# Kernel tuning notes

Measured on AMD Instinct MI355X. Metric: run time of the kernel, lower is better.

The kernel has to match this reference:

```python
import jax, jax.numpy as jnp
import numpy as np

N = 100000   # nodes
E = 1600000  # edges (avg degree 16)
F = 128      # num_features
H = 128      # hidden_channels
L = 3        # mp_layers
C = 40       # num_classes
EPS = 1e-5   # BatchNorm eps


def setup_inputs() -> dict:
    key = jax.random.key(0)
    ks = jax.random.split(key, 6)
    x = jax.random.normal(ks[0], (N, F), dtype=jnp.float32)
    edge_index = jax.random.randint(ks[1], (2, E), 0, N, dtype=jnp.int64)
    # GCNConv weights (F==H so all layers share shape), PyG-style lin + bias
    Ws = jax.random.normal(ks[2], (L, H, H), dtype=jnp.float32) * 0.05
    bs = jnp.zeros((L, H), dtype=jnp.float32)
    # BatchNorm affine params
    gammas = jnp.ones((L, H), dtype=jnp.float32)
    betas = jnp.zeros((L, H), dtype=jnp.float32)
    # output head: skip-concat dim = F + L*H
    W_out = jax.random.normal(ks[3], (F + L * H, C), dtype=jnp.float32) * 0.05
    b_out = jnp.zeros((C,), dtype=jnp.float32)
    return {"x": x, "Ws": Ws, "bs": bs, "gammas": gammas, "betas": betas,
            "W_out": W_out, "b_out": b_out, "edge_index": edge_index}


def reference(x, Ws, bs, gammas, betas, W_out, b_out, edge_index):
    src, dst = edge_index[0], edge_index[1]
    n = x.shape[0]
    # GCN symmetric normalization with self-loops (PyG gcn_norm, add_self_loops=True)
    deg = jax.ops.segment_sum(jnp.ones(src.shape[0], x.dtype), dst, num_segments=n) + 1.0
    dinv = jax.lax.rsqrt(deg)
    edge_norm = (dinv[src] * dinv[dst])[:, None]   # [E,1]
    self_norm = (dinv * dinv)[:, None]             # [N,1] self-loop contribution

    outs = [x]
    h = x
    for i in range(L):
        hw = h @ Ws[i]                                                   # [N,H]
        msg = hw[src] * edge_norm                                        # gather [E,H]
        agg = jax.ops.segment_sum(msg, dst, num_segments=n)              # scatter-add
        agg = agg + hw * self_norm + bs[i]
        # BatchNorm1d in training mode (batch stats, biased variance)
        mu = agg.mean(axis=0)
        var = agg.var(axis=0)
        h = gammas[i] * (agg - mu) * jax.lax.rsqrt(var + EPS) + betas[i]
        outs.append(h)  # dropout p=0.0 -> identity; skip=True collects each layer

    xcat = jnp.concatenate(outs, axis=1)  # [N, F + L*H]
    return xcat @ W_out + b_out
```

## Files before the change

### kernel.cpp

```cpp
#include <hip/hip_runtime.h>

#define NN 100000
#define NE 1600000
#define HD 128
#define NL 3
#define NC 40
#define NCP 48

#define NBK 196
#define NPB 512
#define BSH 9
#define CAP 9216
#define PCAP 13312
#define EPB 6400
#define NBINBLK 250

typedef unsigned int u32;
typedef unsigned short u16;
typedef __attribute__((ext_vector_type(8))) short short8;
typedef __attribute__((ext_vector_type(4))) float f32x4;

__device__ __forceinline__ float b2f(u16 h){
    union{u32 u; float f;} v; v.u = ((u32)h) << 16; return v.f;
}
__device__ __forceinline__ u16 f2b(float f){
    union{float f; u32 u;} v; v.f = f;
    u32 u = v.u;
    u32 r = (u + 0x7FFFu + ((u >> 16) & 1u)) >> 16;
    return (u16)r;
}

__global__ void k_conv_w(const float* __restrict__ Ws, u16* __restrict__ wt,
                         int* __restrict__ gcur, float* __restrict__ stats,
                         u16* __restrict__ hwzero, const float* __restrict__ Wout,
                         u16* __restrict__ woutt){
    int i = blockIdx.x * blockDim.x + threadIdx.x;
    if (i < NBK) gcur[i] = 0;
    if (i < NL * 2 * HD) stats[i] = 0.f;
    if (i < HD) hwzero[i] = 0;
    if (i < (NL + 1) * NCP * HD){
        int li = i / (NCP * HD);
        int r = i % (NCP * HD);
        int n = r / HD;
        int k = r % HD;
        woutt[i] = (n < NC) ? f2b(Wout[(size_t)(li * HD + k) * NC + n]) : (u16)0;
    }
    if (i >= NL * HD * HD) return;
    int l = i / (HD * HD);
    int r = i % (HD * HD);
    int n = r / HD;
    int k = r % HD;
    wt[i] = f2b(Ws[l * HD * HD + k * HD + n]);
}

__launch_bounds__(256)
__global__ void k_bin(const int* __restrict__ src, const int* __restrict__ dst,
                      int* __restrict__ gcur, u32* __restrict__ bb){
    __shared__ int hist[NBK];
    __shared__ int lbase[NBK];
    __shared__ int gbase[NBK];
    __shared__ int cur[NBK];
    __shared__ int wsum[4];
    __shared__ uint2 stage[EPB];
    int tid = threadIdx.x;
    int e0 = blockIdx.x * EPB;
    for (int i = tid; i < NBK; i += 256) hist[i] = 0;
    __syncthreads();
    for (int k = tid; k < EPB; k += 256){
        int d = dst[e0 + k];
        atomicAdd(&hist[d >> BSH], 1);
    }
    __syncthreads();
    {
        int v = (tid < NBK) ? hist[tid] : 0;
        int lane = tid & 63, w = tid >> 6;
        int incl = v;
        #pragma unroll
        for (int dlt = 1; dlt < 64; dlt <<= 1){
            int t = __shfl_up(incl, dlt);
            if (lane >= dlt) incl += t;
        }
        if (lane == 63) wsum[w] = incl;
        __syncthreads();
        if (tid == 0){
            int run = 0;
            #pragma unroll
            for (int j = 0; j < 4; j++){ int t = wsum[j]; wsum[j] = run; run += t; }
        }
        __syncthreads();
        int excl = wsum[w] + incl - v;
        if (tid < NBK){ lbase[tid] = excl; cur[tid] = excl; }
    }
    __syncthreads();
    if (tid < NBK) gbase[tid] = atomicAdd(&gcur[tid], hist[tid]);
    __syncthreads();
    for (int k = tid; k < EPB; k += 256){
        int s = src[e0 + k], d = dst[e0 + k];
        int pos = atomicAdd(&cur[d >> BSH], 1);
        stage[pos] = make_uint2((u32)s, (u32)d);
    }
    __syncthreads();
    for (int k = tid; k < EPB; k += 256){
        uint2 sd = stage[k];
        int b = (int)(sd.y >> BSH);
        int g = gbase[b] + (k - lbase[b]);
        if (g < CAP) bb[(size_t)b * CAP + g] = sd.x | ((sd.y & (NPB - 1)) << 17);
    }
}

__launch_bounds__(512)
__global__ void k_csr(const int* __restrict__ gcur, const u32* __restrict__ bb,
                      int* __restrict__ csr_src, int* __restrict__ offs,
                      int* __restrict__ oend, float* __restrict__ dinv){
    __shared__ int hist[NPB];
    __shared__ int cur[NPB];
    __shared__ int wsum[8];
    __shared__ int totp_s;
    __shared__ int lcsr[PCAP];
    int tid = threadIdx.x;
    int b = blockIdx.x;
    int cnt_b = gcur[b]; if (cnt_b > CAP) cnt_b = CAP;
    const u32* eb = bb + (size_t)b * CAP;
    hist[tid] = 0;
    __syncthreads();
    for (int k = tid; k < cnt_b; k += 512)
        atomicAdd(&hist[eb[k] >> 17], 1);
    __syncthreads();
    int cnt = hist[tid];
    int ps = (1 + cnt + 7) & ~7;
    int lane = tid & 63, w = tid >> 6;
    int incl = ps;
    #pragma unroll
    for (int dlt = 1; dlt < 64; dlt <<= 1){
        int t = __shfl_up(incl, dlt);
        if (lane >= dlt) incl += t;
    }
    if (lane == 63) wsum[w] = incl;
    __syncthreads();
    if (tid == 0){
        int run = 0;
        #pragma unroll
        for (int j = 0; j < 8; j++){ int t = wsum[j]; wsum[j] = run; run += t; }
        totp_s = run;
    }
    __syncthreads();
    int excl = wsum[w] + incl - ps;
    int n = b * NPB + tid;
    offs[n] = b * PCAP + excl;
    oend[n] = b * PCAP + excl + ps;
    if (n < NN) dinv[n] = rsqrtf((float)(cnt + 1));
    cur[tid] = excl + 1;
    int totp = totp_s;
    __syncthreads();
    for (int k = tid; k < totp; k += 512) lcsr[k] = NN;
    __syncthreads();
    lcsr[excl] = (n < NN) ? n : NN;
    __syncthreads();
    for (int k = tid; k < cnt_b; k += 512){
        u32 sd = eb[k];
        int pos = atomicAdd(&cur[sd >> 17], 1);
        lcsr[pos] = (int)(sd & 0x1FFFFu);
    }
    __syncthreads();
    for (int k = tid; k < totp; k += 512)
        csr_src[b * PCAP + k] = lcsr[k];
}

__launch_bounds__(256)
__global__ void k_convgemm(const float* __restrict__ x, const u16* __restrict__ wt,
                           const u16* __restrict__ woutt, const float* __restrict__ bout,
                           const float* __restrict__ dinv, u16* __restrict__ hw,
                           float* __restrict__ out){
    __shared__ u16 wlds[HD * HD];
    __shared__ u16 wolds[NCP * HD];
    __shared__ float bl[NC];
    int tid = threadIdx.x;
    {
        const uint4* g = reinterpret_cast<const uint4*>(wt);
        #pragma unroll
        for (int i = 0; i < 8; i++){
            int lin16 = tid + 256 * i;
            uint4 v = g[lin16];
            int c = lin16 >> 4;
            int addr16 = lin16 ^ (c & 7);
            reinterpret_cast<uint4*>(wlds)[addr16] = v;
        }
    }
    {
        const uint4* g = reinterpret_cast<const uint4*>(woutt);
        #pragma unroll
        for (int i = 0; i < 3; i++){
            int lin16 = tid + 256 * i;
            uint4 v = g[lin16];
            int c = lin16 >> 4;
            int addr16 = lin16 ^ (c & 7);
            reinterpret_cast<uint4*>(wolds)[addr16] = v;
        }
    }
    if (tid < NC) bl[tid] = bout[tid];
    __syncthreads();

    int wv = tid >> 6, lane = tid & 63;
    int row_base = blockIdx.x * 64 + wv * 16;
    int arow = row_base + (lane & 15);
    if (arow >= NN) arow = NN - 1;
    int koff = (lane >> 4) * 8;

    f32x4 accW[8];
    f32x4 accH[3];
    #pragma unroll
    for (int t = 0; t < 8; t++) accW[t] = (f32x4){0.f, 0.f, 0.f, 0.f};
    #pragma unroll
    for (int t = 0; t < 3; t++) accH[t] = (f32x4){0.f, 0.f, 0.f, 0.f};

    #pragma unroll
    for (int kk = 0; kk < 4; kk++){
        int fb = kk * 32 + koff;
        const float4* xr = reinterpret_cast<const float4*>(x + (size_t)arow * HD + fb);
        float4 v0 = xr[0];
        float4 v1 = xr[1];
        short8 a;
        a[0] = (short)f2b(v0.x); a[1] = (short)f2b(v0.y);
        a[2] = (short)f2b(v0.z); a[3] = (short)f2b(v0.w);
        a[4] = (short)f2b(v1.x); a[5] = (short)f2b(v1.y);
        a[6] = (short)f2b(v1.z); a[7] = (short)f2b(v1.w);
        #pragma unroll
        for (int ct = 0; ct < 8; ct++){
            int c = ct * 16 + (lane & 15);
            int addr16 = (c * 16 + kk * 4 + (koff >> 3)) ^ (c & 7);
            short8 b = *reinterpret_cast<const short8*>(wlds + addr16 * 8);
            accW[ct] = __builtin_amdgcn_mfma_f32_16x16x32_bf16(a, b, accW[ct], 0, 0, 0);
        }
        #pragma unroll
        for (int ht = 0; ht < 3; ht++){
            int c = ht * 16 + (lane & 15);
            int addr16 = (c * 16 + kk * 4 + (koff >> 3)) ^ (c & 7);
            short8 b = *reinterpret_cast<const short8*>(wolds + addr16 * 8);
            accH[ht] = __builtin_amdgcn_mfma_f32_16x16x32_bf16(a, b, accH[ht], 0, 0, 0);
        }
    }

    int drow = row_base + (lane >> 4) * 4;
    int dcol = lane & 15;
    float dv[4];
    #pragma unroll
    for (int r = 0; r < 4; r++){
        int rr = drow + r;
        dv[r] = dinv[rr < NN ? rr : NN - 1];
    }
    #pragma unroll
    for (int ct = 0; ct < 8; ct++){
        #pragma unroll
        for (int r = 0; r < 4; r++){
            int rr = drow + r;
            if (rr < NN) hw[rr * HD + ct * 16 + dcol] = f2b(accW[ct][r] * dv[r]);
        }
    }
    #pragma unroll
    for (int ht = 0; ht < 3; ht++){
        int col = ht * 16 + dcol;
        if (col < NC){
            float bv = bl[col];
            #pragma unroll
            for (int r = 0; r < 4; r++){
                int rr = drow + r;
                if (rr < NN) out[(size_t)rr * NC + col] = bv + accH[ht][r];
            }
        }
    }
}

template<bool DO_HW>
__launch_bounds__(256)
__global__ void k_gemmbn(const u16* __restrict__ agg, const float* __restrict__ sums,
                         const float* __restrict__ gamma, const float* __restrict__ beta,
                         const u16* __restrict__ wt, const u16* __restrict__ woutt,
                         const float* __restrict__ dinv, u16* __restrict__ hw,
                         float* __restrict__ out){
    __shared__ u16 wlds[HD * HD];
    __shared__ u16 wolds[NCP * HD];
    __shared__ float Al[HD];
    __shared__ float Cl[HD];
    int tid = threadIdx.x;
    if (DO_HW){
        const uint4* g = reinterpret_cast<const uint4*>(wt);
        #pragma unroll
        for (int i = 0; i < 8; i++){
            int lin16 = tid + 256 * i;
            uint4 v = g[lin16];
            int c = lin16 >> 4;
            int addr16 = lin16 ^ (c & 7);
            reinterpret_cast<uint4*>(wlds)[addr16] = v;
        }
    }
    {
        const uint4* g = reinterpret_cast<const uint4*>(woutt);
        #pragma unroll
        for (int i = 0; i < 3; i++){
            int lin16 = tid + 256 * i;
            uint4 v = g[lin16];
            int c = lin16 >> 4;
            int addr16 = lin16 ^ (c & 7);
            reinterpret_cast<uint4*>(wolds)[addr16] = v;
        }
    }
    if (tid < HD){
        float mu = sums[tid] / (float)NN;
        float var = sums[HD + tid] / (float)NN - mu * mu;
        float inv = rsqrtf(var + 1e-5f);
        float a = gamma[tid] * inv;
        Al[tid] = a;
        Cl[tid] = beta[tid] - mu * a;
    }
    __syncthreads();

    int wv = tid >> 6, lane = tid & 63;
    int row_base = blockIdx.x * 64 + wv * 16;
    int arow = row_base + (lane & 15);
    if (arow >= NN) arow = NN - 1;
    int koff = (lane >> 4) * 8;

    f32x4 accW[8];
    f32x4 accH[3];
    #pragma unroll
    for (int t = 0; t < 8; t++) accW[t] = (f32x4){0.f, 0.f, 0.f, 0.f};
    #pragma unroll
    for (int t = 0; t < 3; t++) accH[t] = (f32x4){0.f, 0.f, 0.f, 0.f};

    #pragma unroll
    for (int kk = 0; kk < 4; kk++){
        int fb = kk * 32 + koff;
        short8 raw = *reinterpret_cast<const short8*>(agg + (size_t)arow * HD + fb);
        f32x4 A0 = *reinterpret_cast<const f32x4*>(&Al[fb]);
        f32x4 A1 = *reinterpret_cast<const f32x4*>(&Al[fb + 4]);
        f32x4 C0 = *reinterpret_cast<const f32x4*>(&Cl[fb]);
        f32x4 C1 = *reinterpret_cast<const f32x4*>(&Cl[fb + 4]);
        short8 a;
        #pragma unroll
        for (int j = 0; j < 4; j++){
            a[j]     = (short)f2b(b2f((u16)raw[j])     * A0[j] + C0[j]);
            a[j + 4] = (short)f2b(b2f((u16)raw[j + 4]) * A1[j] + C1[j]);
        }
        if (DO_HW){
            #pragma unroll
            for (int ct = 0; ct < 8; ct++){
                int c = ct * 16 + (lane & 15);
                int addr16 = (c * 16 + kk * 4 + (koff >> 3)) ^ (c & 7);
                short8 b = *reinterpret_cast<const short8*>(wlds + addr16 * 8);
                accW[ct] = __builtin_amdgcn_mfma_f32_16x16x32_bf16(a, b, accW[ct], 0, 0, 0);
            }
        }
        #pragma unroll
        for (int ht = 0; ht < 3; ht++){
            int c = ht * 16 + (lane & 15);
            int addr16 = (c * 16 + kk * 4 + (koff >> 3)) ^ (c & 7);
            short8 b = *reinterpret_cast<const short8*>(wolds + addr16 * 8);
            accH[ht] = __builtin_amdgcn_mfma_f32_16x16x32_bf16(a, b, accH[ht], 0, 0, 0);
        }
    }

    int drow = row_base + (lane >> 4) * 4;
    int dcol = lane & 15;
    if (DO_HW){
        float dv[4];
        #pragma unroll
        for (int r = 0; r < 4; r++){
            int rr = drow + r;
            dv[r] = dinv[rr < NN ? rr : NN - 1];
        }
        #pragma unroll
        for (int ct = 0; ct < 8; ct++){
            #pragma unroll
            for (int r = 0; r < 4; r++){
                int rr = drow + r;
                if (rr < NN) hw[rr * HD + ct * 16 + dcol] = f2b(accW[ct][r] * dv[r]);
            }
        }
    }
    #pragma unroll
    for (int ht = 0; ht < 3; ht++){
        int col = ht * 16 + dcol;
        if (col < NC){
            #pragma unroll
            for (int r = 0; r < 4; r++){
                int rr = drow + r;
                if (rr < NN) out[(size_t)rr * NC + col] += accH[ht][r];
            }
        }
    }
}

__launch_bounds__(256)
__global__ void k_agg(const u16* __restrict__ hw, const int* __restrict__ offs,
                      const int* __restrict__ oend, const int* __restrict__ csr_src,
                      const float* __restrict__ dinv, const float* __restrict__ bias,
                      u16* __restrict__ agg, float* __restrict__ sums){
    __shared__ float redS[4][HD];
    __shared__ float redQ[4][HD];
    int tid = threadIdx.x;
    int lane = tid & 63;
    int wv = tid >> 6;
    int f0 = lane * 2;
    float b0 = bias[f0], b1 = bias[f0 + 1];
    float s0 = 0.f, s1 = 0.f, q0 = 0.f, q1 = 0.f;
    int n0 = (blockIdx.x * 4 + wv) * 16;
    const u32* hw32 = reinterpret_cast<const u32*>(hw);

    for (int k = 0; k < 16; k++){
        int n = n0 + k;
        if (n >= NN) break;
        float a0 = 0.f, a1 = 0.f, c0 = 0.f, c1 = 0.f;
        int e = offs[n], e1 = oend[n];
        int rem = e1 - e;
        while (rem > 0){
            int win = rem < 64 ? rem : 64;
            int idxv = csr_src[e + lane];
            int nch = win >> 3;
            u32 va[8], vb[8];

            #pragma unroll
            for (int j = 0; j < 8; j++){
                u32 uid = (u32)__builtin_amdgcn_readlane(idxv, j);
                va[j] = hw32[(size_t)(uid << 6) + (u32)lane];
            }
            for (int c = 1; c < nch; c++){
                if (c & 1){
                    #pragma unroll
                    for (int j = 0; j < 8; j++){
                        u32 uid = (u32)__builtin_amdgcn_readlane(idxv, c * 8 + j);
                        vb[j] = hw32[(size_t)(uid << 6) + (u32)lane];
                    }
                    #pragma unroll
                    for (int j = 0; j < 8; j++){
                        union{u32 u; float f;} L, H;
                        L.u = va[j] << 16; H.u = va[j] & 0xFFFF0000u;
                        a0 += L.f; a1 += H.f;
                    }
                } else {
                    #pragma unroll
                    for (int j = 0; j < 8; j++){
                        u32 uid = (u32)__builtin_amdgcn_readlane(idxv, c * 8 + j);
                        va[j] = hw32[(size_t)(uid << 6) + (u32)lane];
                    }
                    #pragma unroll
                    for (int j = 0; j < 8; j++){
                        union{u32 u; float f;} L, H;
                        L.u = vb[j] << 16; H.u = vb[j] & 0xFFFF0000u;
                        c0 += L.f; c1 += H.f;
                    }
                }
            }
            if (nch & 1){
                #pragma unroll
                for (int j = 0; j < 8; j++){
                    union{u32 u; float f;} L, H;
                    L.u = va[j] << 16; H.u = va[j] & 0xFFFF0000u;
                    a0 += L.f; a1 += H.f;
                }
            } else {
                #pragma unroll
                for (int j = 0; j < 8; j++){
                    union{u32 u; float f;} L, H;
                    L.u = vb[j] << 16; H.u = vb[j] & 0xFFFF0000u;
                    c0 += L.f; c1 += H.f;
                }
            }
            e += win; rem -= win;
        }
        float di = dinv[n];
        a0 = (a0 + c0) * di + b0;
        a1 = (a1 + c1) * di + b1;
        u32 o = ((u32)f2b(a1) << 16) | (u32)f2b(a0);
        *reinterpret_cast<u32*>(agg + (size_t)n * HD + f0) = o;
        s0 += a0; s1 += a1; q0 += a0 * a0; q1 += a1 * a1;
    }

    redS[wv][f0] = s0; redS[wv][f0 + 1] = s1;
    redQ[wv][f0] = q0; redQ[wv][f0 + 1] = q1;
    __syncthreads();
    if (tid < HD){
        float ts = redS[0][tid] + redS[1][tid] + redS[2][tid] + redS[3][tid];
        float tq = redQ[0][tid] + redQ[1][tid] + redQ[2][tid] + redQ[3][tid];
        atomicAdd(&sums[tid], ts);
        atomicAdd(&sums[HD + tid], tq);
    }
}

extern "C" void kernel_launch(void* const* d_in, const int* in_sizes, int n_in,
                              void* d_out, int out_size, void* d_ws, size_t ws_size,
                              hipStream_t stream){
    const float* x      = (const float*)d_in[0];
    const float* Ws     = (const float*)d_in[1];
    const float* bs     = (const float*)d_in[2];
    const float* gammas = (const float*)d_in[3];
    const float* betas  = (const float*)d_in[4];
    const float* W_out  = (const float*)d_in[5];
    const float* b_out  = (const float*)d_in[6];
    const int*   ei     = (const int*)d_in[7];
    const int* src = ei;
    const int* dst = ei + NE;
    float* out = (float*)d_out;

    char* ws = (char*)d_ws;
    size_t off = 0;
    auto alloc = [&](size_t bytes) -> char* {
        char* p = ws + off;
        off += (bytes + 255) & ~(size_t)255;
        return p;
    };
    u16*   hw       = (u16*)alloc((size_t)(NN + 1) * HD * 2);
    u16*   aggb     = (u16*)alloc((size_t)NN * HD * 2);
    u16*   wt       = (u16*)alloc((size_t)NL * HD * HD * 2);
    u16*   woutt    = (u16*)alloc((size_t)(NL + 1) * NCP * HD * 2);
    float* dinv     = (float*)alloc((size_t)NN * 4);
    int*   offs     = (int*)alloc((size_t)(NBK * NPB) * 4);
    int*   oend     = (int*)alloc((size_t)(NBK * NPB) * 4);
    int*   gcur     = (int*)alloc((size_t)NBK * 4);
    int*   csr_src  = (int*)alloc(((size_t)NBK * PCAP + 256) * 4);
    float* stats    = (float*)alloc((size_t)NL * 2 * HD * 4);

    u32* bb = (u32*)aggb;

    k_conv_w<<<(NL * HD * HD + 255) / 256, 256, 0, stream>>>(Ws, wt, gcur, stats,
                                                             hw + (size_t)NN * HD,
                                                             W_out, woutt);
    k_bin<<<NBINBLK, 256, 0, stream>>>(src, dst, gcur, bb);
    k_csr<<<NBK, 512, 0, stream>>>(gcur, bb, csr_src, offs, oend, dinv);

    k_convgemm<<<(NN + 63) / 64, 256, 0, stream>>>(x, wt, woutt, b_out, dinv, hw, out);

    for (int l = 0; l < NL; l++){
        k_agg<<<(NN + 63) / 64, 256, 0, stream>>>(hw, offs, oend, csr_src, dinv,
                                                  bs + (size_t)l * HD, aggb,
                                                  stats + (size_t)l * 2 * HD);
        if (l < NL - 1){
            k_gemmbn<true><<<(NN + 63) / 64, 256, 0, stream>>>(
                aggb, stats + (size_t)l * 2 * HD, gammas + (size_t)l * HD,
                betas + (size_t)l * HD, wt + (size_t)(l + 1) * HD * HD,
                woutt + (size_t)(l + 1) * NCP * HD, dinv, hw, out);
        } else {
            k_gemmbn<false><<<(NN + 63) / 64, 256, 0, stream>>>(
                aggb, stats + (size_t)l * 2 * HD, gammas + (size_t)l * HD,
                betas + (size_t)l * HD, nullptr,
                woutt + (size_t)(l + 1) * NCP * HD, dinv, nullptr, out);
        }
    }
}
```

Baseline: 420.6 us.

## Quantize transformed node features to int8 with per-row scales for aggregation

The GEMM epilogues now quantize each row of h@W (scaled by dinv) to int8 using a per-row absmax scale, and store the per-row inverse scale separately. The aggregation kernel gathers 2-byte pairs instead of 4-byte bf16 pairs and dequantizes with a per-neighbour scale broadcast via readlane. This halves the gather traffic in the memory-bound scatter/gather step. In exchange it costs a cross-lane max reduction in the epilogue, an extra scale load per edge, and reduced precision (int8 vs bf16) that may affect accuracy tolerance.

```diff
diff --git a/kernel.cpp b/kernel.cpp
--- a/kernel.cpp
+++ b/kernel.cpp
@@ -17,6 +17,7 @@
 
 typedef unsigned int u32;
 typedef unsigned short u16;
+typedef signed char i8;
 typedef __attribute__((ext_vector_type(8))) short short8;
 typedef __attribute__((ext_vector_type(4))) float f32x4;
 
@@ -32,12 +33,13 @@
 
 __global__ void k_conv_w(const float* __restrict__ Ws, u16* __restrict__ wt,
                          int* __restrict__ gcur, float* __restrict__ stats,
-                         u16* __restrict__ hwzero, const float* __restrict__ Wout,
-                         u16* __restrict__ woutt){
+                         u32* __restrict__ hw8zero, float* __restrict__ invscale,
+                         const float* __restrict__ Wout, u16* __restrict__ woutt){
     int i = blockIdx.x * blockDim.x + threadIdx.x;
     if (i < NBK) gcur[i] = 0;
     if (i < NL * 2 * HD) stats[i] = 0.f;
-    if (i < HD) hwzero[i] = 0;
+    if (i < 32) hw8zero[i] = 0;
+    if (i == 0) invscale[NN] = 0.f;
     if (i < (NL + 1) * NCP * HD){
         int li = i / (NCP * HD);
         int r = i % (NCP * HD);
@@ -166,11 +168,27 @@
         csr_src[b * PCAP + k] = lcsr[k];
 }
 
+#define EPI_INT8(ACC, DVR, RR) { \
+    float m_ = 0.f; \
+    _Pragma("unroll") \
+    for (int ct_ = 0; ct_ < 8; ct_++) m_ = fmaxf(m_, fabsf(ACC[ct_][RR##_r])); \
+    _Pragma("unroll") \
+    for (int off_ = 1; off_ < 16; off_ <<= 1) m_ = fmaxf(m_, __shfl_xor(m_, off_)); \
+    float s_ = (m_ > 0.f) ? 127.0f / m_ : 0.f; \
+    if (RR < NN){ \
+        _Pragma("unroll") \
+        for (int ct_ = 0; ct_ < 8; ct_++){ \
+            int q_ = (int)rintf(ACC[ct_][RR##_r] * s_); \
+            hw8[(size_t)RR * HD + ct_ * 16 + dcol] = (i8)q_; \
+        } \
+        if (dcol == 0) invscale[RR] = m_ * DVR * (1.0f / 127.0f); \
+    } }
+
 __launch_bounds__(256)
 __global__ void k_convgemm(const float* __restrict__ x, const u16* __restrict__ wt,
                            const u16* __restrict__ woutt, const float* __restrict__ bout,
-                           const float* __restrict__ dinv, u16* __restrict__ hw,
-                           float* __restrict__ out){
+                           const float* __restrict__ dinv, i8* __restrict__ hw8,
+                           float* __restrict__ invscale, float* __restrict__ out){
     __shared__ u16 wlds[HD * HD];
     __shared__ u16 wolds[NCP * HD];
     __shared__ float bl[NC];
@@ -242,19 +260,11 @@
 
     int drow = row_base + (lane >> 4) * 4;
     int dcol = lane & 15;
-    float dv[4];
-    #pragma unroll
-    for (int r = 0; r < 4; r++){
-        int rr = drow + r;
-        dv[r] = dinv[rr < NN ? rr : NN - 1];
-    }
-    #pragma unroll
-    for (int ct = 0; ct < 8; ct++){
-        #pragma unroll
-        for (int r = 0; r < 4; r++){
-            int rr = drow + r;
-            if (rr < NN) hw[rr * HD + ct * 16 + dcol] = f2b(accW[ct][r] * dv[r]);
-        }
+    #pragma unroll
+    for (int rr_r = 0; rr_r < 4; rr_r++){
+        int rr = drow + rr_r;
+        float dvr = dinv[rr < NN ? rr : NN - 1];
+        EPI_INT8(accW, dvr, rr)
     }
     #pragma unroll
     for (int ht = 0; ht < 3; ht++){
@@ -275,8 +285,8 @@
 __global__ void k_gemmbn(const u16* __restrict__ agg, const float* __restrict__ sums,
                          const float* __restrict__ gamma, const float* __restrict__ beta,
                          const u16* __restrict__ wt, const u16* __restrict__ woutt,
-                         const float* __restrict__ dinv, u16* __restrict__ hw,
-                         float* __restrict__ out){
+                         const float* __restrict__ dinv, i8* __restrict__ hw8,
+                         float* __restrict__ invscale, float* __restrict__ out){
     __shared__ u16 wlds[HD * HD];
     __shared__ u16 wolds[NCP * HD];
     __shared__ float Al[HD];
@@ -362,19 +372,11 @@
     int drow = row_base + (lane >> 4) * 4;
     int dcol = lane & 15;
     if (DO_HW){
-        float dv[4];
-        #pragma unroll
-        for (int r = 0; r < 4; r++){
-            int rr = drow + r;
-            dv[r] = dinv[rr < NN ? rr : NN - 1];
-        }
-        #pragma unroll
-        for (int ct = 0; ct < 8; ct++){
-            #pragma unroll
-            for (int r = 0; r < 4; r++){
-                int rr = drow + r;
-                if (rr < NN) hw[rr * HD + ct * 16 + dcol] = f2b(accW[ct][r] * dv[r]);
-            }
+        #pragma unroll
+        for (int rr_r = 0; rr_r < 4; rr_r++){
+            int rr = drow + rr_r;
+            float dvr = dinv[rr < NN ? rr : NN - 1];
+            EPI_INT8(accW, dvr, rr)
         }
     }
     #pragma unroll
@@ -390,11 +392,24 @@
     }
 }
 
+#define G8(bufv, bufs, c) { _Pragma("unroll") \
+    for (int j = 0; j < 8; j++){ \
+        u32 uid = (u32)__builtin_amdgcn_readlane(idxv, (c) * 8 + j); \
+        bufs[j] = __int_as_float(__builtin_amdgcn_readlane(scv, (c) * 8 + j)); \
+        bufv[j] = (u32)hw16[(size_t)uid * 64 + (u32)lane]; } }
+
+#define A8(bufv, bufs, x0, x1) { _Pragma("unroll") \
+    for (int j = 0; j < 8; j++){ \
+        int q0 = (int)(i8)(bufv[j] & 0xFF); \
+        int q1 = (int)(i8)(bufv[j] >> 8); \
+        x0 += (float)q0 * bufs[j]; x1 += (float)q1 * bufs[j]; } }
+
 __launch_bounds__(256)
-__global__ void k_agg(const u16* __restrict__ hw, const int* __restrict__ offs,
-                      const int* __restrict__ oend, const int* __restrict__ csr_src,
-                      const float* __restrict__ dinv, const float* __restrict__ bias,
-                      u16* __restrict__ agg, float* __restrict__ sums){
+__global__ void k_agg(const i8* __restrict__ hw8, const float* __restrict__ invscale,
+                      const int* __restrict__ offs, const int* __restrict__ oend,
+                      const int* __restrict__ csr_src, const float* __restrict__ dinv,
+                      const float* __restrict__ bias, u16* __restrict__ agg,
+                      float* __restrict__ sums){
     __shared__ float redS[4][HD];
     __shared__ float redQ[4][HD];
     int tid = threadIdx.x;
@@ -404,7 +419,7 @@
     float b0 = bias[f0], b1 = bias[f0 + 1];
     float s0 = 0.f, s1 = 0.f, q0 = 0.f, q1 = 0.f;
     int n0 = (blockIdx.x * 4 + wv) * 16;
-    const u32* hw32 = reinterpret_cast<const u32*>(hw);
+    const u16* hw16 = reinterpret_cast<const u16*>(hw8);
 
     for (int k = 0; k < 16; k++){
         int n = n0 + k;
@@ -415,55 +430,26 @@
         while (rem > 0){
             int win = rem < 64 ? rem : 64;
             int idxv = csr_src[e + lane];
+            idxv = min(max(idxv, 0), NN);
+            int scv = __float_as_int(invscale[idxv]);
             int nch = win >> 3;
             u32 va[8], vb[8];
-
-            #pragma unroll
-            for (int j = 0; j < 8; j++){
-                u32 uid = (u32)__builtin_amdgcn_readlane(idxv, j);
-                va[j] = hw32[(size_t)(uid << 6) + (u32)lane];
-            }
+            float sa[8], sb[8];
+
+            G8(va, sa, 0)
             for (int c = 1; c < nch; c++){
                 if (c & 1){
-                    #pragma unroll
-                    for (int j = 0; j < 8; j++){
-                        u32 uid = (u32)__builtin_amdgcn_readlane(idxv, c * 8 + j);
-                        vb[j] = hw32[(size_t)(uid << 6) + (u32)lane];
-                    }
-                    #pragma unroll
-                    for (int j = 0; j < 8; j++){
-                        union{u32 u; float f;} L, H;
-                        L.u = va[j] << 16; H.u = va[j] & 0xFFFF0000u;
-                        a0 += L.f; a1 += H.f;
-                    }
+                    G8(vb, sb, c)
+                    A8(va, sa, a0, a1)
                 } else {
-                    #pragma unroll
-                    for (int j = 0; j < 8; j++){
-                        u32 uid = (u32)__builtin_amdgcn_readlane(idxv, c * 8 + j);
-                        va[j] = hw32[(size_t)(uid << 6) + (u32)lane];
-                    }
-                    #pragma unroll
-                    for (int j = 0; j < 8; j++){
-                        union{u32 u; float f;} L, H;
-                        L.u = vb[j] << 16; H.u = vb[j] & 0xFFFF0000u;
-                        c0 += L.f; c1 += H.f;
-                    }
+                    G8(va, sa, c)
+                    A8(vb, sb, c0, c1)
                 }
             }
             if (nch & 1){
-                #pragma unroll
-                for (int j = 0; j < 8; j++){
-                    union{u32 u; float f;} L, H;
-                    L.u = va[j] << 16; H.u = va[j] & 0xFFFF0000u;
-                    a0 += L.f; a1 += H.f;
-                }
+                A8(va, sa, a0, a1)
             } else {
-                #pragma unroll
-                for (int j = 0; j < 8; j++){
-                    union{u32 u; float f;} L, H;
-                    L.u = vb[j] << 16; H.u = vb[j] & 0xFFFF0000u;
-                    c0 += L.f; c1 += H.f;
-                }
+                A8(vb, sb, c0, c1)
             }
             e += win; rem -= win;
         }
@@ -508,7 +494,8 @@
         off += (bytes + 255) & ~(size_t)255;
         return p;
     };
-    u16*   hw       = (u16*)alloc((size_t)(NN + 1) * HD * 2);
+    i8*    hw8      = (i8*)alloc((size_t)(NN + 1) * HD);
+    float* invscale = (float*)alloc((size_t)(NN + 1) * 4);
     u16*   aggb     = (u16*)alloc((size_t)NN * HD * 2);
     u16*   wt       = (u16*)alloc((size_t)NL * HD * HD * 2);
     u16*   woutt    = (u16*)alloc((size_t)(NL + 1) * NCP * HD * 2);
@@ -521,28 +508,28 @@
 
     u32* bb = (u32*)aggb;
 
-    k_conv_w<<<(NL * HD * HD + 255) / 256, 256, 0, stream>>>(Ws, wt, gcur, stats,
-                                                             hw + (size_t)NN * HD,
-                                                             W_out, woutt);
+    k_conv_w<<<(NL * HD * HD + 255) / 256, 256, 0, stream>>>(
+        Ws, wt, gcur, stats, (u32*)(hw8 + (size_t)NN * HD), invscale, W_out, woutt);
     k_bin<<<NBINBLK, 256, 0, stream>>>(src, dst, gcur, bb);
     k_csr<<<NBK, 512, 0, stream>>>(gcur, bb, csr_src, offs, oend, dinv);
 
-    k_convgemm<<<(NN + 63) / 64, 256, 0, stream>>>(x, wt, woutt, b_out, dinv, hw, out);
+    k_convgemm<<<(NN + 63) / 64, 256, 0, stream>>>(x, wt, woutt, b_out, dinv,
+                                                   hw8, invscale, out);
 
     for (int l = 0; l < NL; l++){
-        k_agg<<<(NN + 63) / 64, 256, 0, stream>>>(hw, offs, oend, csr_src, dinv,
-                                                  bs + (size_t)l * HD, aggb,
+        k_agg<<<(NN + 63) / 64, 256, 0, stream>>>(hw8, invscale, offs, oend, csr_src,
+                                                  dinv, bs + (size_t)l * HD, aggb,
                                                   stats + (size_t)l * 2 * HD);
         if (l < NL - 1){
             k_gemmbn<true><<<(NN + 63) / 64, 256, 0, stream>>>(
                 aggb, stats + (size_t)l * 2 * HD, gammas + (size_t)l * HD,
                 betas + (size_t)l * HD, wt + (size_t)(l + 1) * HD * HD,
-                woutt + (size_t)(l + 1) * NCP * HD, dinv, hw, out);
+                woutt + (size_t)(l + 1) * NCP * HD, dinv, hw8, invscale, out);
         } else {
             k_gemmbn<false><<<(NN + 63) / 64, 256, 0, stream>>>(
                 aggb, stats + (size_t)l * 2 * HD, gammas + (size_t)l * HD,
                 betas + (size_t)l * HD, nullptr,
-                woutt + (size_t)(l + 1) * NCP * HD, dinv, nullptr, out);
-        }
-    }
-}
+                woutt + (size_t)(l + 1) * NCP * HD, dinv, nullptr, invscale, out);
+        }
+    }
+}
```

Result: faster. 394.0 us, median of 2 (-6.3%).
